# Kernel tuning notes

Measured on AMD Instinct MI355X. Metric: run time of the kernel, lower is better.

Reference implementation:

```python
import jax, jax.numpy as jnp
import numpy as np

ALPHA = 1.0
CROP_LEN = 256


def setup_inputs() -> dict:
    key = jax.random.key(0)
    k1, k2, k3, k4 = jax.random.split(key, 4)
    B, L1, L2 = 512, 16384, 2048
    conv_len = L1 - L2 + 1  # 14337
    return {
        "pred_astf": jax.random.normal(k1, (B, L1), jnp.float32),
        "true_astf": jax.random.normal(k2, (B, L1), jnp.float32),
        "egf": jax.random.normal(k3, (B, L2), jnp.float32),
        "target_waveform": jax.random.normal(k4, (B, conv_len), jnp.float32),
    }


def _center_crop(x, crop_len):
    L = x.shape[1]
    start = (L - crop_len) // 2
    return jax.lax.dynamic_slice_in_dim(x, start, crop_len, axis=1)


def reference(pred_astf, true_astf, egf, target_waveform):
    B, L1 = pred_astf.shape
    L_target = target_waveform.shape[1]

    # ASTF MSE
    loss_astf = jnp.mean((pred_astf - true_astf) ** 2)

    # Grouped conv1d (per-example valid cross-correlation of pred with egf).
    # torch F.conv1d == lax conv (both are correlation, no kernel flip).
    conv = jax.lax.conv_general_dilated(
        pred_astf[None],          # (1, B, L1)
        egf[:, None, :],          # (B, 1, L2)
        window_strides=(1,),
        padding='VALID',
        feature_group_count=B,
        dimension_numbers=('NCH', 'OIH', 'NCH'),
    )[0]                          # (B, conv_len)
    conv_len = conv.shape[1]

    # FFT cross-correlation to find per-sample alignment shift
    n = 2 * conv_len - 1
    target_padded = jnp.pad(target_waveform, ((0, 0), (0, conv_len - L_target)))
    cc = jnp.fft.irfft(
        jnp.fft.rfft(conv, n=n) * jnp.conj(jnp.fft.rfft(target_padded, n=n)),
        n=n,
    )
    shifts = jnp.argmax(cc, axis=1) - (conv_len - 1)  # (B,)

    # _batch_roll(conv, -shifts): out[b, j] = conv[b, (j + shifts[b]) % L]
    idx = (jnp.arange(conv_len)[None, :] + shifts[:, None]) % conv_len
    conv_aligned = jnp.take_along_axis(conv, idx, axis=1)

    conv_cropped = _center_crop(conv_aligned, CROP_LEN)
    target_cropped = _center_crop(target_waveform, CROP_LEN)
    loss_conv = jnp.mean((conv_cropped - target_cropped) ** 2)

    total_loss = loss_astf + ALPHA * loss_conv
    return total_loss, loss_astf, loss_conv
```

## Files before the change

### kernel.cpp

```cpp
#include <hip/hip_runtime.h>

#define BB     512
#define L1     16384
#define L2     2048
#define CL     14337
#define NCC    28673
#define PADL   14336
#define CROW   14340
#define CROP   256
#define CSTART 7040
#define TLEN   14337
#define FM     16384
#define LOGM   14

#define NPAD  17408
#define IDX(i) ((i) + ((i) >> 4))

__device__ __forceinline__ int rev4_14(int x) {
  int b = (int)(__brev((unsigned)x) >> 18);
  return ((b & 0x1555) << 1) | ((b >> 1) & 0x1555);
}

__device__ __forceinline__ unsigned int fkey(float f) {
  unsigned int b = __float_as_uint(f);
  return b ^ ((b & 0x80000000u) ? 0xFFFFFFFFu : 0x80000000u);
}

__device__ __forceinline__ float blockReduceSum256(float v) {
  #pragma unroll
  for (int o = 32; o > 0; o >>= 1) v += __shfl_down(v, o, 64);
  __shared__ float sws[4];
  if ((threadIdx.x & 63) == 0) sws[threadIdx.x >> 6] = v;
  __syncthreads();
  float r = 0.f;
  if (threadIdx.x == 0) r = sws[0] + sws[1] + sws[2] + sws[3];
  return r;
}

__device__ __forceinline__ float2 cmul(const float2 w, const float2 u) {
  return make_float2(w.x * u.x - w.y * u.y, w.x * u.y + w.y * u.x);
}
__device__ __forceinline__ float2 cmulc(const float2 x, const float2 w) {
  return make_float2(w.x * x.x + w.y * x.y, w.x * x.y - w.y * x.x);
}

__device__ __forceinline__ void bf4_dif(float2& x0, float2& x1, float2& x2, float2& x3) {
  float t0r = x0.x + x2.x, t0i = x0.y + x2.y;
  float t1r = x1.x + x3.x, t1i = x1.y + x3.y;
  float t2r = x0.x - x2.x, t2i = x0.y - x2.y;
  float t3r = x1.y - x3.y, t3i = x3.x - x1.x;
  x0 = make_float2(t0r + t1r, t0i + t1i);
  x1 = make_float2(t2r + t3r, t2i + t3i);
  x2 = make_float2(t0r - t1r, t0i - t1i);
  x3 = make_float2(t2r - t3r, t2i - t3i);
}

__device__ __forceinline__ void bf4_dit(float2& x0, float2& x1, float2& x2, float2& x3) {
  float s0r = x0.x + x2.x, s0i = x0.y + x2.y;
  float s1r = x0.x - x2.x, s1i = x0.y - x2.y;
  float s2r = x1.x + x3.x, s2i = x1.y + x3.y;
  float s3r = x3.y - x1.y, s3i = x1.x - x3.x;
  x0 = make_float2(s0r + s2r, s0i + s2i);
  x1 = make_float2(s1r + s3r, s1i + s3i);
  x2 = make_float2(s0r - s2r, s0i - s2i);
  x3 = make_float2(s1r - s3r, s1i - s3i);
}

template <int S>
__device__ __forceinline__ void fft_dif4_pair(float2* A, const float2* __restrict__ tw,
                                              int tid) {
  __syncthreads();
  constexpr int Q  = 1 << (2 * S - 2);
  constexpr int TS = 12 - 2 * S;
  #pragma unroll 1
  for (int r = 0; r < 2; ++r) {
    const int bf = (r << 9) | tid;
    const int jq = bf & (Q - 1);
    const int hi = bf >> (2 * S - 2);
    const int base = (hi << (2 * S + 2)) | jq;
    float2 x[4][4];
    #pragma unroll
    for (int a = 0; a < 4; ++a)
      #pragma unroll
      for (int b = 0; b < 4; ++b)
        x[a][b] = A[IDX(base + (a << (2 * S)) + (b << (2 * S - 2)))];
    #pragma unroll
    for (int b = 0; b < 4; ++b) {
      bf4_dif(x[0][b], x[1][b], x[2][b], x[3][b]);
      const int jt = (b * Q + jq) << TS;
      x[1][b] = cmul(tw[jt],     x[1][b]);
      x[2][b] = cmul(tw[2 * jt], x[2][b]);
      x[3][b] = cmul(tw[3 * jt], x[3][b]);
    }
    const int jt2 = jq << (14 - 2 * S);
    const float2 v1 = tw[jt2], v2 = tw[2 * jt2], v3 = tw[3 * jt2];
    #pragma unroll
    for (int a = 0; a < 4; ++a) {
      bf4_dif(x[a][0], x[a][1], x[a][2], x[a][3]);
      x[a][1] = cmul(v1, x[a][1]);
      x[a][2] = cmul(v2, x[a][2]);
      x[a][3] = cmul(v3, x[a][3]);
    }
    #pragma unroll
    for (int a = 0; a < 4; ++a)
      #pragma unroll
      for (int b = 0; b < 4; ++b)
        A[IDX(base + (a << (2 * S)) + (b << (2 * S - 2)))] = x[a][b];
  }
}

__device__ __forceinline__ void fft_dif4_last(float2* A, int tid) {
  __syncthreads();
  for (int r = 0; r < 8; ++r) {
    const int i0 = ((r << 9) | tid) << 2;
    const int p0 = IDX(i0), p1 = IDX(i0 + 1), p2 = IDX(i0 + 2), p3 = IDX(i0 + 3);
    float2 x0 = A[p0], x1 = A[p1], x2 = A[p2], x3 = A[p3];
    bf4_dif(x0, x1, x2, x3);
    A[p0] = x0; A[p1] = x1; A[p2] = x2; A[p3] = x3;
  }
}

__device__ __forceinline__ void fft_dit4_first(float2* A, int tid) {
  __syncthreads();
  for (int r = 0; r < 8; ++r) {
    const int i0 = ((r << 9) | tid) << 2;
    const int p0 = IDX(i0), p1 = IDX(i0 + 1), p2 = IDX(i0 + 2), p3 = IDX(i0 + 3);
    float2 x0 = A[p0], x1 = A[p1], x2 = A[p2], x3 = A[p3];
    bf4_dit(x0, x1, x2, x3);
    A[p0] = x0; A[p1] = x1; A[p2] = x2; A[p3] = x3;
  }
}

template <int S>
__device__ __forceinline__ void fft_dit4_pair(float2* A, const float2* __restrict__ tw,
                                              int tid) {
  __syncthreads();
  constexpr int M = 1 << (2 * S);
  #pragma unroll 1
  for (int r = 0; r < 2; ++r) {
    const int bf = (r << 9) | tid;
    const int jq = bf & (M - 1);
    const int hi = bf >> (2 * S);
    const int base = (hi << (2 * S + 4)) | jq;
    float2 x[4][4];
    #pragma unroll
    for (int a = 0; a < 4; ++a)
      #pragma unroll
      for (int b = 0; b < 4; ++b)
        x[a][b] = A[IDX(base + (b << (2 * S + 2)) + (a << (2 * S)))];
    const int jt = jq << (12 - 2 * S);
    const float2 w1 = tw[jt], w2 = tw[2 * jt], w3 = tw[3 * jt];
    #pragma unroll
    for (int b = 0; b < 4; ++b) {
      x[1][b] = cmulc(x[1][b], w1);
      x[2][b] = cmulc(x[2][b], w2);
      x[3][b] = cmulc(x[3][b], w3);
      bf4_dit(x[0][b], x[1][b], x[2][b], x[3][b]);
    }
    #pragma unroll
    for (int a = 0; a < 4; ++a) {
      const int jt2 = (a * M + jq) << (10 - 2 * S);
      x[a][1] = cmulc(x[a][1], tw[jt2]);
      x[a][2] = cmulc(x[a][2], tw[2 * jt2]);
      x[a][3] = cmulc(x[a][3], tw[3 * jt2]);
      bf4_dit(x[a][0], x[a][1], x[a][2], x[a][3]);
    }
    #pragma unroll
    for (int a = 0; a < 4; ++a)
      #pragma unroll
      for (int b = 0; b < 4; ++b)
        A[IDX(base + (b << (2 * S + 2)) + (a << (2 * S)))] = x[a][b];
  }
}

__device__ __forceinline__ void fft_dif4(float2* A, const float2* __restrict__ tw, int tid) {
  fft_dif4_pair<6>(A, tw, tid);
  fft_dif4_pair<4>(A, tw, tid);
  fft_dif4_pair<2>(A, tw, tid);
  fft_dif4_last(A, tid);
  __syncthreads();
}

__device__ __forceinline__ void fft_dit4_inv(float2* A, const float2* __restrict__ tw, int tid) {
  fft_dit4_first(A, tid);
  fft_dit4_pair<1>(A, tw, tid);
  fft_dit4_pair<3>(A, tw, tid);
  fft_dit4_pair<5>(A, tw, tid);
  __syncthreads();
}


__global__ void init_kernel(unsigned long long* best, float* acc) {
  int i = blockIdx.x * blockDim.x + threadIdx.x;
  if (i < BB) best[i] = 0ull;
  if (i < 4)  acc[i]  = 0.f;
}

__global__ void twid_kernel(float2* tw, float2* w32) {
  int i = blockIdx.x * 256 + threadIdx.x;
  if (i < FM) {
    double a = -2.0 * 3.14159265358979323846 * (double)i / (double)FM;
    tw[i] = make_float2((float)cos(a), (float)sin(a));
  }
  if (i < 8192) {
    double a = -2.0 * 3.14159265358979323846 * (double)i / (double)(2 * FM);
    w32[i] = make_float2((float)cos(a), (float)sin(a));
  }
}

__global__ void astf_kernel(const float* __restrict__ p, const float* __restrict__ t,
                            float* __restrict__ acc) {
  int gid = blockIdx.x * blockDim.x + threadIdx.x;
  int stride = gridDim.x * blockDim.x;
  const float4* p4 = (const float4*)p;
  const float4* t4 = (const float4*)t;
  const int n4 = (BB * L1) / 4;
  float s = 0.f;
  for (int i = gid; i < n4; i += stride) {
    float4 a = p4[i], b = t4[i];
    float dx = a.x - b.x, dy = a.y - b.y, dz = a.z - b.z, dw = a.w - b.w;
    s += dx * dx + dy * dy + dz * dz + dw * dw;
  }
  s = blockReduceSum256(s);
  if (threadIdx.x == 0) atomicAdd(&acc[0], s);
}

__global__ __launch_bounds__(512, 2) void convfft_kernel(const float* __restrict__ pred,
                                                         const float* __restrict__ egf,
                                                         const float2* __restrict__ tw,
                                                         float* __restrict__ convbuf) {
  __shared__ float2 A[NPAD];
  const int tid = threadIdx.x;
  const int b = blockIdx.x;
  const float* pb = pred + (size_t)b * L1;
  const float* eb = egf  + (size_t)b * L2;

  for (int i = tid; i < FM; i += 512)
    A[IDX(i)] = make_float2(pb[i], (i < L2) ? eb[i] : 0.f);

  fft_dif4(A, tw, tid);

  for (int rr = 0; rr < 16; ++rr) {
    const int k = tid * 16 + rr;
    if (k == 0) {
      float2 z0 = A[IDX(0)];
      A[IDX(0)] = make_float2(z0.x * z0.y, 0.f);
      const int p = IDX(2);
      float2 zn = A[p];
      A[p] = make_float2(zn.x * zn.y, 0.f);
    } else {
      const int p = IDX(rev4_14(k)), q = IDX(rev4_14(FM - k));
      float2 z1 = A[p], z2 = A[q];
      float pr = 0.5f * (z1.x + z2.x), pi = 0.5f * (z1.y - z2.y);
      float er = 0.5f * (z1.y + z2.y), ei = 0.5f * (z2.x - z1.x);
      float sr = pr * er + pi * ei;
      float si = pi * er - pr * ei;
      A[p] = make_float2(sr, si);
      A[q] = make_float2(sr, -si);
    }
  }

  fft_dit4_inv(A, tw, tid);

  float* cr = convbuf + (size_t)b * CROW;
  const float sc = 1.f / (float)FM;
  for (int i = tid; i < CL; i += 512) cr[i] = A[IDX(i)].x * sc;
}

__global__ __launch_bounds__(512, 2) void ccfft_kernel(const float* __restrict__ convbuf,
                                                       const float* __restrict__ target,
                                                       const float2* __restrict__ tw,
                                                       const float2* __restrict__ w32,
                                                       float4* __restrict__ spec,
                                                       unsigned long long* __restrict__ best) {
  __shared__ float2 A[NPAD];
  __shared__ unsigned long long sbest[8];
  const int tid = threadIdx.x;
  float4* sp = spec + (size_t)blockIdx.x * 8192;

  for (int half = 0; half < 2; ++half) {
    const int b = blockIdx.x * 2 + half;
    const float* cr = convbuf + (size_t)b * CROW;
    const float* tr = target  + (size_t)b * TLEN;

    for (int i = tid; i < 7168; i += 512)
      A[IDX(i)] = *(const float2*)(cr + 2 * i);
    for (int i = 7168 + tid; i < FM; i += 512) {
      float re = (i == 7168) ? cr[14336] : 0.f;
      A[IDX(i)] = make_float2(re, 0.f);
    }
    fft_dif4(A, tw, tid);

    #pragma unroll 1
    for (int rr = 0; rr < 16; ++rr) {
      const int k = tid * 16 + rr;
      const int s = (rr << 9) | tid;
      float2 ya, yb;
      if (k == 0) { ya = A[IDX(0)]; yb = A[IDX(2)]; }
      else        { ya = A[IDX(rev4_14(k))]; yb = A[IDX(rev4_14(FM - k))]; }
      sp[s] = make_float4(ya.x, ya.y, yb.x, yb.y);
    }
    __syncthreads();

    for (int i = tid; i < FM; i += 512) {
      int g = 2 * i;
      float re = (g     < TLEN) ? tr[g]     : 0.f;
      float im = (g + 1 < TLEN) ? tr[g + 1] : 0.f;
      A[IDX(i)] = make_float2(re, im);
    }
    fft_dif4(A, tw, tid);

    #pragma unroll 1
    for (int rr = 0; rr < 16; ++rr) {
      const int k = tid * 16 + rr;
      const int s = (rr << 9) | tid;
      const float4 y4 = sp[s];
      if (k == 0) {
        float2 yc0 = make_float2(y4.x, y4.y), yt0 = A[IDX(0)];
        float X0 = yc0.x + yc0.y, XM = yc0.x - yc0.y;
        float T0 = yt0.x + yt0.y, TM = yt0.x - yt0.y;
        float C0 = X0 * T0, CM = XM * TM;
        A[IDX(0)] = make_float2(0.5f * (C0 + CM), 0.5f * (C0 - CM));
        float2 yc = make_float2(y4.z, y4.w), yt = A[IDX(2)];
        float cr8 = yc.x * yt.x + yc.y * yt.y;
        float ci8 = yc.x * yt.y - yc.y * yt.x;
        A[IDX(2)] = make_float2(cr8, -ci8);
      } else {
        const int p = IDX(rev4_14(k)), q = IDX(rev4_14(FM - k));
        const float2 w = w32[k];
        float2 ya = make_float2(y4.x, y4.y), yb = make_float2(y4.z, y4.w);
        float xer = 0.5f * (ya.x + yb.x), xei = 0.5f * (ya.y - yb.y);
        float dr  = 0.5f * (ya.x - yb.x), di  = 0.5f * (ya.y + yb.y);
        float xo_r = di, xo_i = -dr;
        float wxr = w.x * xo_r - w.y * xo_i, wxi = w.x * xo_i + w.y * xo_r;
        float Xkr = xer + wxr, Xki = xei + wxi;
        float Xmr = xer - wxr, Xmi = -(xei - wxi);
        float2 ta = A[p], tb = A[q];
        float ter = 0.5f * (ta.x + tb.x), tei = 0.5f * (ta.y - tb.y);
        float er2 = 0.5f * (ta.x - tb.x), ei2 = 0.5f * (ta.y + tb.y);
        float to_r = ei2, to_i = -er2;
        float twr = w.x * to_r - w.y * to_i, twi = w.x * to_i + w.y * to_r;
        float Tkr = ter + twr, Tki = tei + twi;
        float Tmr = ter - twr, Tmi = -(tei - twi);
        float Ckr = Xkr * Tkr + Xki * Tki, Cki = Xki * Tkr - Xkr * Tki;
        float Cmr = Xmr * Tmr + Xmi * Tmi, Cmi = Xmi * Tmr - Xmr * Tmi;
        float aer = 0.5f * (Ckr + Cmr), aei = 0.5f * (Cki - Cmi);
        float bdr = 0.5f * (Ckr - Cmr), bdi = 0.5f * (Cki + Cmi);
        float cor_ = w.x * bdr + w.y * bdi, coi = w.x * bdi - w.y * bdr;
        A[p] = make_float2(aer - coi, aei + cor_);
        float a2r = 0.5f * (Cmr + Ckr), a2i = 0.5f * (Cmi - Cki);
        float d2r = 0.5f * (Cmr - Ckr), d2i = 0.5f * (Cmi + Cki);
        float c2r = -(w.x * d2r - w.y * d2i), c2i = -(w.x * d2i + w.y * d2r);
        A[q] = make_float2(a2r - c2i, a2i + c2r);
      }
    }

    fft_dit4_inv(A, tw, tid);

    unsigned long long pk = 0ull;
    for (int i = tid; i < FM; i += 512) {
      float2 v = A[IDX(i)];
      int j0 = 2 * i, j1 = 2 * i + 1;
      if (j0 <= 14336) {
        unsigned long long p = ((unsigned long long)fkey(v.x) << 32)
                             | (unsigned long long)(0xFFFFFFFFu - (unsigned)j0);
        if (p > pk) pk = p;
      } else if (j0 >= 18432) {
        unsigned long long p = ((unsigned long long)fkey(v.x) << 32)
                             | (unsigned long long)(0xFFFFFFFFu - (unsigned)(j0 - 4095));
        if (p > pk) pk = p;
      }
      if (j1 <= 14336) {
        unsigned long long p = ((unsigned long long)fkey(v.y) << 32)
                             | (unsigned long long)(0xFFFFFFFFu - (unsigned)j1);
        if (p > pk) pk = p;
      } else if (j1 >= 18432) {
        unsigned long long p = ((unsigned long long)fkey(v.y) << 32)
                             | (unsigned long long)(0xFFFFFFFFu - (unsigned)(j1 - 4095));
        if (p > pk) pk = p;
      }
    }
    #pragma unroll
    for (int o = 32; o > 0; o >>= 1) {
      unsigned long long q = __shfl_down(pk, o, 64);
      if (q > pk) pk = q;
    }
    if ((tid & 63) == 0) sbest[tid >> 6] = pk;
    __syncthreads();
    if (tid == 0) {
      #pragma unroll
      for (int i = 1; i < 8; ++i) if (sbest[i] > pk) pk = sbest[i];
      best[b] = pk;
    }
    __syncthreads();
  }
}


__device__ __forceinline__ void taps4(float* acc, const float4 a, const float4 b,
                                      const float4 e) {
  acc[0] = fmaf(a.x, e.x, acc[0]); acc[0] = fmaf(a.y, e.y, acc[0]);
  acc[0] = fmaf(a.z, e.z, acc[0]); acc[0] = fmaf(a.w, e.w, acc[0]);
  acc[1] = fmaf(a.y, e.x, acc[1]); acc[1] = fmaf(a.z, e.y, acc[1]);
  acc[1] = fmaf(a.w, e.z, acc[1]); acc[1] = fmaf(b.x, e.w, acc[1]);
  acc[2] = fmaf(a.z, e.x, acc[2]); acc[2] = fmaf(a.w, e.y, acc[2]);
  acc[2] = fmaf(b.x, e.z, acc[2]); acc[2] = fmaf(b.y, e.w, acc[2]);
  acc[3] = fmaf(a.w, e.x, acc[3]); acc[3] = fmaf(b.x, e.y, acc[3]);
  acc[3] = fmaf(b.y, e.z, acc[3]); acc[3] = fmaf(b.z, e.w, acc[3]);
}

__device__ __forceinline__ float4 gload4(const float* __restrict__ cr, int g) {
  if (g >= 0 && g + 3 < CL) return *(const float4*)(cr + g);
  float4 v;
  int g0 = min(max(g,     0), CL - 1);
  int g1 = min(max(g + 1, 0), CL - 1);
  int g2 = min(max(g + 2, 0), CL - 1);
  int g3 = min(max(g + 3, 0), CL - 1);
  v.x = (g     >= 0 && g     < CL) ? cr[g0] : 0.f;
  v.y = (g + 1 >= 0 && g + 1 < CL) ? cr[g1] : 0.f;
  v.z = (g + 2 >= 0 && g + 2 < CL) ? cr[g2] : 0.f;
  v.w = (g + 3 >= 0 && g + 3 < CL) ? cr[g3] : 0.f;
  return v;
}

__global__ __launch_bounds__(256) void conv_kernel(const float* __restrict__ pred,
                                                   const float* __restrict__ egf,
                                                   float* __restrict__ convbuf) {
  const int b = blockIdx.y;
  const int x = blockIdx.x;
  const int tid = threadIdx.x;
  const float* pb = pred + (size_t)b * L1;
  const float* eg = egf  + (size_t)b * L2;
  float* cr = convbuf + (size_t)b * CROW;

  if (x == 7) {
    float s = 0.f;
    const int k0 = tid * 8;
    #pragma unroll
    for (int j = 0; j < 8; ++j) s += pb[PADL + k0 + j] * eg[k0 + j];
    s = blockReduceSum256(s);
    if (tid == 0) cr[PADL] = s;
    return;
  }

  const int m = x * 2048 + tid * 8;
  const float* cp = pb + m;
  float accA[4] = {0.f,0.f,0.f,0.f};
  float accB[4] = {0.f,0.f,0.f,0.f};
  float4 w0 = *(const float4*)(cp);
  float4 w1 = *(const float4*)(cp + 4);
  float4 w2 = *(const float4*)(cp + 8);

  #pragma unroll 4
  for (int k = 0; k < L2 - 4; k += 4) {
    const float4 e  = *(const float4*)(eg + k);
    const float4 nx = *(const float4*)(cp + k + 12);
    taps4(accA, w0, w1, e);
    taps4(accB, w1, w2, e);
    w0 = w1; w1 = w2; w2 = nx;
  }
  {
    const float4 e = *(const float4*)(eg + (L2 - 4));
    taps4(accA, w0, w1, e);
    taps4(accB, w1, w2, e);
  }

  *(float4*)(cr + m)     = make_float4(accA[0], accA[1], accA[2], accA[3]);
  *(float4*)(cr + m + 4) = make_float4(accB[0], accB[1], accB[2], accB[3]);
}

__global__ __launch_bounds__(256) void cc_kernel(const float* __restrict__ convbuf,
                                                 const float* __restrict__ target,
                                                 unsigned long long* __restrict__ best) {
  __shared__ unsigned long long sbest[4];
  const int b   = blockIdx.y;
  const int m0  = blockIdx.x * 2048;
  const int tid = threadIdx.x;
  const float* cr = convbuf + (size_t)b * CROW;
  const float* tr = target  + (size_t)b * TLEN;
  const int m    = m0 + tid * 8;
  const int gofs = m - PADL;

  float accA[4] = {0.f,0.f,0.f,0.f};
  float accB[4] = {0.f,0.f,0.f,0.f};

  const int t1raw = PADL - m0;
  const int t1    = t1raw > 0 ? t1raw : 0;
  const int t2    = PADL + CL - m0 - 2047;
  int tIntHi      = (t2 - 16) & ~3;
  if (tIntHi > 14332) tIntHi = 14332;
  if (tIntHi < t1)    tIntHi = t1;
  int e0 = (t1raw - 2047) > 0 ? ((t1raw - 2047) & ~3) : 0;
  const int eH = min(TLEN, NCC - m0);

  if (e0 < t1) {
    float4 w0 = gload4(cr, gofs + e0);
    float4 w1 = gload4(cr, gofs + e0 + 4);
    float4 w2 = gload4(cr, gofs + e0 + 8);
    #pragma unroll 2
    for (int t = e0; t < t1; t += 4) {
      const float4 e  = *(const float4*)(tr + t);
      const float4 nx = gload4(cr, gofs + t + 12);
      taps4(accA, w0, w1, e);
      taps4(accB, w1, w2, e);
      w0 = w1; w1 = w2; w2 = nx;
    }
  }

  if (t1 < tIntHi) {
    const float* cp = cr + gofs;
    float4 w0 = *(const float4*)(cp + t1);
    float4 w1 = *(const float4*)(cp + t1 + 4);
    float4 w2 = *(const float4*)(cp + t1 + 8);
    #pragma unroll 4
    for (int t = t1; t < tIntHi; t += 4) {
      const float4 e  = *(const float4*)(tr + t);
      const float4 nx = *(const float4*)(cp + t + 12);
      taps4(accA, w0, w1, e);
      taps4(accB, w1, w2, e);
      w0 = w1; w1 = w2; w2 = nx;
    }
  }

  if (tIntHi < eH) {
    float4 w0 = gload4(cr, gofs + tIntHi);
    float4 w1 = gload4(cr, gofs + tIntHi + 4);
    float4 w2 = gload4(cr, gofs + tIntHi + 8);
    #pragma unroll 2
    for (int t = tIntHi; t < eH; t += 4) {
      float4 e;
      e.x = (t     < TLEN) ? tr[t]     : 0.f;
      e.y = (t + 1 < TLEN) ? tr[t + 1] : 0.f;
      e.z = (t + 2 < TLEN) ? tr[t + 2] : 0.f;
      e.w = (t + 3 < TLEN) ? tr[t + 3] : 0.f;
      const float4 nx = gload4(cr, gofs + t + 12);
      taps4(accA, w0, w1, e);
      taps4(accB, w1, w2, e);
      w0 = w1; w1 = w2; w2 = nx;
    }
  }

  unsigned long long pk = 0ull;
  #pragma unroll
  for (int j = 0; j < 4; ++j) {
    int mm = m + j;
    if (mm < NCC) {
      int np = (mm >= PADL) ? (mm - PADL) : (mm + CL);
      unsigned long long p = ((unsigned long long)fkey(accA[j]) << 32)
                           | (unsigned long long)(0xFFFFFFFFu - (unsigned)np);
      if (p > pk) pk = p;
    }
    mm = m + 4 + j;
    if (mm < NCC) {
      int np = (mm >= PADL) ? (mm - PADL) : (mm + CL);
      unsigned long long p = ((unsigned long long)fkey(accB[j]) << 32)
                           | (unsigned long long)(0xFFFFFFFFu - (unsigned)np);
      if (p > pk) pk = p;
    }
  }
  #pragma unroll
  for (int o = 32; o > 0; o >>= 1) {
    unsigned long long q = __shfl_down(pk, o, 64);
    if (q > pk) pk = q;
  }
  if ((tid & 63) == 0) sbest[tid >> 6] = pk;
  __syncthreads();
  if (tid == 0) {
    #pragma unroll
    for (int i = 1; i < 4; ++i) if (sbest[i] > pk) pk = sbest[i];
    atomicMax(best + b, pk);
  }
}

__global__ void closs_kernel(const float* __restrict__ convbuf,
                             const float* __restrict__ target,
                             const unsigned long long* __restrict__ best,
                             float* __restrict__ acc) {
  const int b = blockIdx.x;
  const int np = (int)(0xFFFFFFFFu - (unsigned)(best[b] & 0xFFFFFFFFull));
  const int shift = np - PADL;
  const int jj = CSTART + threadIdx.x;
  int pos = jj + shift;
  if (pos < 0) pos += CL; else if (pos >= CL) pos -= CL;
  float d = convbuf[(size_t)b * CROW + pos] - target[(size_t)b * TLEN + jj];
  float s = blockReduceSum256(d * d);
  if (threadIdx.x == 0) atomicAdd(&acc[1], s);
}

__global__ void fin_kernel(const float* __restrict__ acc, float* __restrict__ out) {
  if (threadIdx.x == 0 && blockIdx.x == 0) {
    float la = acc[0] / (float)((long)BB * L1);
    float lc = acc[1] / (float)(BB * CROP);
    out[0] = la + lc;
    out[1] = la;
    out[2] = lc;
  }
}


extern "C" void kernel_launch(void* const* d_in, const int* in_sizes, int n_in,
                              void* d_out, int out_size, void* d_ws, size_t ws_size,
                              hipStream_t stream) {
  (void)in_sizes; (void)n_in; (void)out_size;
  const float* pred   = (const float*)d_in[0];
  const float* truea  = (const float*)d_in[1];
  const float* egf    = (const float*)d_in[2];
  const float* target = (const float*)d_in[3];
  float* out = (float*)d_out;

  char* ws = (char*)d_ws;
  const size_t off_best = (size_t)BB * CROW * 4;
  const size_t off_acc  = off_best + (size_t)BB * 8;
  const size_t off_tw   = off_acc + 256;
  const size_t off_w32  = off_tw + (size_t)FM * 8;
  const size_t off_spec = off_w32 + (size_t)8192 * 8;
  const size_t needed   = off_spec + (size_t)256 * FM * 8;

  float* convbuf            = (float*)ws;
  unsigned long long* best  = (unsigned long long*)(ws + off_best);
  float* acc                = (float*)(ws + off_acc);
  float2* tw                = (float2*)(ws + off_tw);
  float2* w32               = (float2*)(ws + off_w32);
  float4* spec              = (float4*)(ws + off_spec);

  init_kernel<<<2, 256, 0, stream>>>(best, acc);
  astf_kernel<<<1024, 256, 0, stream>>>(pred, truea, acc);

  if (ws_size >= needed) {
    twid_kernel<<<64, 256, 0, stream>>>(tw, w32);
    convfft_kernel<<<BB, 512, 0, stream>>>(pred, egf, tw, convbuf);
    ccfft_kernel<<<BB / 2, 512, 0, stream>>>(convbuf, target, tw, w32, spec, best);
  } else {
    conv_kernel<<<dim3(8, BB), 256, 0, stream>>>(pred, egf, convbuf);
    cc_kernel<<<dim3(15, BB), 256, 0, stream>>>(convbuf, target, best);
  }

  closs_kernel<<<dim3(BB), 256, 0, stream>>>(convbuf, target, best, acc);
  fin_kernel<<<1, 64, 0, stream>>>(acc, out);
}
```

Measured before the change: 275.4 us.

## Fuse convolution FFT and cross-correlation FFT into a single per-pair kernel

Merges the convolution FFT kernel into the cross-correlation FFT kernel, so each block computes the convolution for its two batch rows and then runs the correlation FFT on them in the same launch. This removes one kernel launch and the boundary between the two stages. Conv output is still written to global memory and read back after a block barrier. It also precomputes padded shared-memory base indices so the per-element index math is cheaper. The trade-off is that the conv stage now runs on only 256 blocks instead of 512, which reduces parallelism for that stage.

```diff
diff --git a/kernel.cpp b/kernel.cpp
--- a/kernel.cpp
+++ b/kernel.cpp
@@ -15,6 +15,7 @@
 
 #define NPAD  17408
 #define IDX(i) ((i) + ((i) >> 4))
+#define PADOFF(o) ((o) + ((o) >> 4))
 
 __device__ __forceinline__ int rev4_14(int x) {
   int b = (int)(__brev((unsigned)x) >> 18);
@@ -77,13 +78,13 @@
     const int bf = (r << 9) | tid;
     const int jq = bf & (Q - 1);
     const int hi = bf >> (2 * S - 2);
-    const int base = (hi << (2 * S + 2)) | jq;
+    const int pb = IDX((hi << (2 * S + 2)) | jq);
     float2 x[4][4];
     #pragma unroll
     for (int a = 0; a < 4; ++a)
       #pragma unroll
       for (int b = 0; b < 4; ++b)
-        x[a][b] = A[IDX(base + (a << (2 * S)) + (b << (2 * S - 2)))];
+        x[a][b] = A[pb + PADOFF((a << (2 * S)) + (b << (2 * S - 2)))];
     #pragma unroll
     for (int b = 0; b < 4; ++b) {
       bf4_dif(x[0][b], x[1][b], x[2][b], x[3][b]);
@@ -105,29 +106,27 @@
     for (int a = 0; a < 4; ++a)
       #pragma unroll
       for (int b = 0; b < 4; ++b)
-        A[IDX(base + (a << (2 * S)) + (b << (2 * S - 2)))] = x[a][b];
+        A[pb + PADOFF((a << (2 * S)) + (b << (2 * S - 2)))] = x[a][b];
   }
 }
 
 __device__ __forceinline__ void fft_dif4_last(float2* A, int tid) {
   __syncthreads();
   for (int r = 0; r < 8; ++r) {
-    const int i0 = ((r << 9) | tid) << 2;
-    const int p0 = IDX(i0), p1 = IDX(i0 + 1), p2 = IDX(i0 + 2), p3 = IDX(i0 + 3);
-    float2 x0 = A[p0], x1 = A[p1], x2 = A[p2], x3 = A[p3];
+    const int p0 = IDX((((r << 9) | tid) << 2));
+    float2 x0 = A[p0], x1 = A[p0 + 1], x2 = A[p0 + 2], x3 = A[p0 + 3];
     bf4_dif(x0, x1, x2, x3);
-    A[p0] = x0; A[p1] = x1; A[p2] = x2; A[p3] = x3;
+    A[p0] = x0; A[p0 + 1] = x1; A[p0 + 2] = x2; A[p0 + 3] = x3;
   }
 }
 
 __device__ __forceinline__ void fft_dit4_first(float2* A, int tid) {
   __syncthreads();
   for (int r = 0; r < 8; ++r) {
-    const int i0 = ((r << 9) | tid) << 2;
-    const int p0 = IDX(i0), p1 = IDX(i0 + 1), p2 = IDX(i0 + 2), p3 = IDX(i0 + 3);
-    float2 x0 = A[p0], x1 = A[p1], x2 = A[p2], x3 = A[p3];
+    const int p0 = IDX((((r << 9) | tid) << 2));
+    float2 x0 = A[p0], x1 = A[p0 + 1], x2 = A[p0 + 2], x3 = A[p0 + 3];
     bf4_dit(x0, x1, x2, x3);
-    A[p0] = x0; A[p1] = x1; A[p2] = x2; A[p3] = x3;
+    A[p0] = x0; A[p0 + 1] = x1; A[p0 + 2] = x2; A[p0 + 3] = x3;
   }
 }
 
@@ -141,13 +140,13 @@
     const int bf = (r << 9) | tid;
     const int jq = bf & (M - 1);
     const int hi = bf >> (2 * S);
-    const int base = (hi << (2 * S + 4)) | jq;
+    const int pb = IDX((hi << (2 * S + 4)) | jq);
     float2 x[4][4];
     #pragma unroll
     for (int a = 0; a < 4; ++a)
       #pragma unroll
       for (int b = 0; b < 4; ++b)
-        x[a][b] = A[IDX(base + (b << (2 * S + 2)) + (a << (2 * S)))];
+        x[a][b] = A[pb + PADOFF((b << (2 * S + 2)) + (a << (2 * S)))];
     const int jt = jq << (12 - 2 * S);
     const float2 w1 = tw[jt], w2 = tw[2 * jt], w3 = tw[3 * jt];
     #pragma unroll
@@ -169,7 +168,7 @@
     for (int a = 0; a < 4; ++a)
       #pragma unroll
       for (int b = 0; b < 4; ++b)
-        A[IDX(base + (b << (2 * S + 2)) + (a << (2 * S)))] = x[a][b];
+        A[pb + PADOFF((b << (2 * S + 2)) + (a << (2 * S)))] = x[a][b];
   }
 }
 
@@ -225,54 +224,14 @@
   if (threadIdx.x == 0) atomicAdd(&acc[0], s);
 }
 
-__global__ __launch_bounds__(512, 2) void convfft_kernel(const float* __restrict__ pred,
+__global__ __launch_bounds__(512, 2) void pipefft_kernel(const float* __restrict__ pred,
                                                          const float* __restrict__ egf,
+                                                         const float* __restrict__ target,
                                                          const float2* __restrict__ tw,
-                                                         float* __restrict__ convbuf) {
-  __shared__ float2 A[NPAD];
-  const int tid = threadIdx.x;
-  const int b = blockIdx.x;
-  const float* pb = pred + (size_t)b * L1;
-  const float* eb = egf  + (size_t)b * L2;
-
-  for (int i = tid; i < FM; i += 512)
-    A[IDX(i)] = make_float2(pb[i], (i < L2) ? eb[i] : 0.f);
-
-  fft_dif4(A, tw, tid);
-
-  for (int rr = 0; rr < 16; ++rr) {
-    const int k = tid * 16 + rr;
-    if (k == 0) {
-      float2 z0 = A[IDX(0)];
-      A[IDX(0)] = make_float2(z0.x * z0.y, 0.f);
-      const int p = IDX(2);
-      float2 zn = A[p];
-      A[p] = make_float2(zn.x * zn.y, 0.f);
-    } else {
-      const int p = IDX(rev4_14(k)), q = IDX(rev4_14(FM - k));
-      float2 z1 = A[p], z2 = A[q];
-      float pr = 0.5f * (z1.x + z2.x), pi = 0.5f * (z1.y - z2.y);
-      float er = 0.5f * (z1.y + z2.y), ei = 0.5f * (z2.x - z1.x);
-      float sr = pr * er + pi * ei;
-      float si = pi * er - pr * ei;
-      A[p] = make_float2(sr, si);
-      A[q] = make_float2(sr, -si);
-    }
-  }
-
-  fft_dit4_inv(A, tw, tid);
-
-  float* cr = convbuf + (size_t)b * CROW;
-  const float sc = 1.f / (float)FM;
-  for (int i = tid; i < CL; i += 512) cr[i] = A[IDX(i)].x * sc;
-}
-
-__global__ __launch_bounds__(512, 2) void ccfft_kernel(const float* __restrict__ convbuf,
-                                                       const float* __restrict__ target,
-                                                       const float2* __restrict__ tw,
-                                                       const float2* __restrict__ w32,
-                                                       float4* __restrict__ spec,
-                                                       unsigned long long* __restrict__ best) {
+                                                         const float2* __restrict__ w32,
+                                                         float* convbuf,
+                                                         float4* __restrict__ spec,
+                                                         unsigned long long* __restrict__ best) {
   __shared__ float2 A[NPAD];
   __shared__ unsigned long long sbest[8];
   const int tid = threadIdx.x;
@@ -280,8 +239,41 @@
 
   for (int half = 0; half < 2; ++half) {
     const int b = blockIdx.x * 2 + half;
-    const float* cr = convbuf + (size_t)b * CROW;
+    const float* pb = pred + (size_t)b * L1;
+    const float* eb = egf  + (size_t)b * L2;
+    float* cr       = convbuf + (size_t)b * CROW;
     const float* tr = target  + (size_t)b * TLEN;
+
+    for (int i = tid; i < FM; i += 512)
+      A[IDX(i)] = make_float2(pb[i], (i < L2) ? eb[i] : 0.f);
+
+    fft_dif4(A, tw, tid);
+
+    for (int rr = 0; rr < 16; ++rr) {
+      const int k = tid * 16 + rr;
+      if (k == 0) {
+        float2 z0 = A[IDX(0)];
+        A[IDX(0)] = make_float2(z0.x * z0.y, 0.f);
+        const int p = IDX(2);
+        float2 zn = A[p];
+        A[p] = make_float2(zn.x * zn.y, 0.f);
+      } else {
+        const int p = IDX(rev4_14(k)), q = IDX(rev4_14(FM - k));
+        float2 z1 = A[p], z2 = A[q];
+        float pr = 0.5f * (z1.x + z2.x), pi = 0.5f * (z1.y - z2.y);
+        float er = 0.5f * (z1.y + z2.y), ei = 0.5f * (z2.x - z1.x);
+        float sr = pr * er + pi * ei;
+        float si = pi * er - pr * ei;
+        A[p] = make_float2(sr, si);
+        A[q] = make_float2(sr, -si);
+      }
+    }
+
+    fft_dit4_inv(A, tw, tid);
+
+    const float sc = 1.f / (float)FM;
+    for (int i = tid; i < CL; i += 512) cr[i] = A[IDX(i)].x * sc;
+    __syncthreads();
 
     for (int i = tid; i < 7168; i += 512)
       A[IDX(i)] = *(const float2*)(cr + 2 * i);
@@ -628,8 +620,8 @@
 
   if (ws_size >= needed) {
     twid_kernel<<<64, 256, 0, stream>>>(tw, w32);
-    convfft_kernel<<<BB, 512, 0, stream>>>(pred, egf, tw, convbuf);
-    ccfft_kernel<<<BB / 2, 512, 0, stream>>>(convbuf, target, tw, w32, spec, best);
+    pipefft_kernel<<<BB / 2, 512, 0, stream>>>(pred, egf, target, tw, w32,
+                                               convbuf, spec, best);
   } else {
     conv_kernel<<<dim3(8, BB), 256, 0, stream>>>(pred, egf, convbuf);
     cc_kernel<<<dim3(15, BB), 256, 0, stream>>>(convbuf, target, best);
```

After: 250.1 us. -9.2%, faster.
